# Optimization experiments

Hardware: AMD Instinct MI355X
Metric: run time of the kernel (lower is better)

## Reference

```python
import jax, jax.numpy as jnp
import numpy as np

B = 4          # batch_size (config.batch_size)
N = 17000      # num_prots (nodes per graph)
F_IN = 256     # num_features
C = 128        # out_channels
E = 2176000    # num edges (avg degree 32)
NODES = B * N


def _gcn_layer(x, W, b, src, dst, n):
    """PyG GCNConv: add self-loops, sym-normalized aggregation, then bias.
    out[i] = sum_{j->i} d_j^{-1/2} d_i^{-1/2} (x_j W) + d_i^{-1} (x_i W) + b
    with d = degree(dst) + 1 (self loop)."""
    h = x @ W  # [n, C]
    deg = jax.ops.segment_sum(jnp.ones(src.shape[0], x.dtype), dst, num_segments=n) + 1.0
    dinv = jax.lax.rsqrt(deg)  # [n]
    coef = dinv[src] * dinv[dst]                      # [E]
    agg = jax.ops.segment_sum(h[src] * coef[:, None], dst, num_segments=n)
    agg = agg + h * (dinv * dinv)[:, None]            # self-loop term
    return agg + b


def setup_inputs() -> dict:
    key = jax.random.key(0)
    ks = jax.random.split(key, 16)

    def glorot(k, shape):
        fan_in, fan_out = shape[0], shape[1]
        s = jnp.sqrt(6.0 / (fan_in + fan_out))
        return jax.random.uniform(k, shape, jnp.float32, -s, s)

    inp = {
        "x": jax.random.normal(ks[0], (NODES, F_IN), jnp.float32),
        "edge_index": jax.random.randint(ks[1], (2, E), 0, NODES, jnp.int32),
        "protein_mask": jax.random.randint(ks[2], (B, N), 0, 2, jnp.int32),
        "W1": glorot(ks[3], (F_IN, C)), "b1": jnp.zeros((C,), jnp.float32),
        "W2": glorot(ks[4], (C, C)),    "b2": jnp.zeros((C,), jnp.float32),
        "W3": glorot(ks[5], (C, C)),    "b3": jnp.zeros((C,), jnp.float32),
        "lw1": glorot(ks[6], (C, 256)), "lb1": jnp.zeros((256,), jnp.float32),
        "lw2": glorot(ks[7], (256, 64)), "lb2": jnp.zeros((64,), jnp.float32),
        "lw3": glorot(ks[8], (64, 16)),  "lb3": jnp.zeros((16,), jnp.float32),
        "lw4": glorot(ks[9], (16, 1)),   "lb4": jnp.zeros((1,), jnp.float32),
    }
    return inp


def reference(x, edge_index, protein_mask, W1, b1, W2, b2, W3, b3,
              lw1, lb1, lw2, lb2, lw3, lb3, lw4, lb4):
    src, dst = edge_index[0], edge_index[1]
    h1 = jax.nn.relu(_gcn_layer(x, W1, b1, src, dst, NODES))   # [NODES, C]
    h2 = jax.nn.relu(_gcn_layer(h1, W2, b2, src, dst, NODES))
    h3 = jax.nn.relu(_gcn_layer(h2, W3, b3, src, dst, NODES))
    s = (h1 + h2 + h3).reshape(B, N, C)                        # residual sum
    mask = protein_mask.astype(jnp.float32)                    # [B, N]
    pooled = jnp.einsum('bn,bnc->bc', mask, s)                 # masked bmm pool [B, C]
    z = jax.nn.relu(pooled @ lw1 + lb1)
    z = jax.nn.relu(z @ lw2 + lb2)
    z = jax.nn.relu(z @ lw3 + lb3)
    return z @ lw4 + lb4                                       # [B, 1]
```

## Files before the change

kernel.cpp:

```cpp
#include <hip/hip_runtime.h>
#include <hip/hip_bf16.h>
#include <cstdint>

#define F_IN 256
#define C 128
#define NBUK_MAX 320
#define CHUNK 4096
#define CAP 12288

typedef short bf8_t __attribute__((ext_vector_type(8)));
typedef float f4_t  __attribute__((ext_vector_type(4)));

static inline size_t align256(size_t x) { return (x + 255) & ~(size_t)255; }

static __device__ inline unsigned pack_bf16(float a, float b) {
    __hip_bfloat162 h = __float22bfloat162_rn(make_float2(a, b));
    return *(unsigned*)&h;
}

static __device__ inline bf8_t pack8(float4 u0, float4 u1) {
    union { unsigned u[4]; bf8_t v; } r;
    r.u[0] = pack_bf16(u0.x, u0.y);
    r.u[1] = pack_bf16(u0.z, u0.w);
    r.u[2] = pack_bf16(u1.x, u1.y);
    r.u[3] = pack_bf16(u1.z, u1.w);
    return r.v;
}

__global__ __launch_bounds__(256) void part_gemm1_kernel(
        const int* __restrict__ src, const int* __restrict__ dst,
        int* __restrict__ cntb, int* __restrict__ ebuf, int E, int nblk_part,
        const float* __restrict__ X, const __hip_bfloat16* __restrict__ Wsw,
        __hip_bfloat16* __restrict__ G, int M) {
    __shared__ __align__(16) char smem[36864];
    const int tid = threadIdx.x;

    if ((int)blockIdx.x < nblk_part) {
        int* hist = (int*)smem;
        int* base = hist + NBUK_MAX;
        int* gbase = base + NBUK_MAX;
        int2* stage = (int2*)(smem + 4096);
        const int e0 = blockIdx.x * CHUNK;
        const int cnt = min(CHUNK, E - e0);

        for (int i = tid; i < NBUK_MAX; i += 256) hist[i] = 0;
        __syncthreads();

        int2 ev[CHUNK / 256];
        int mo[CHUNK / 256];
#pragma unroll
        for (int k = 0; k < CHUNK / 256; ++k) {
            int e = e0 + k * 256 + tid;
            if (e < E) {
                int2 v;
                v.x = src[e];
                v.y = dst[e];
                ev[k] = v;
                mo[k] = atomicAdd(&hist[v.y >> 8], 1);
            }
        }
        __syncthreads();
        if (tid < 64) {
            int acc[5];
            int s = 0;
#pragma unroll
            for (int j = 0; j < 5; ++j) {
                acc[j] = s;
                s += hist[tid * 5 + j];
            }
            int tot = s;
#pragma unroll
            for (int d = 1; d < 64; d <<= 1) {
                int o = __shfl_up(tot, d);
                if (tid >= d) tot += o;
            }
            int excl = tot - s;
#pragma unroll
            for (int j = 0; j < 5; ++j) base[tid * 5 + j] = excl + acc[j];
        }
        __syncthreads();
        for (int i = tid; i < NBUK_MAX; i += 256) {
            int h = hist[i];
            gbase[i] = h ? atomicAdd(&cntb[i], h) : 0;
        }
        __syncthreads();
#pragma unroll
        for (int k = 0; k < CHUNK / 256; ++k) {
            int e = e0 + k * 256 + tid;
            if (e < E) stage[base[ev[k].y >> 8] + mo[k]] = ev[k];
        }
        __syncthreads();
        for (int i = tid; i < cnt; i += 256) {
            int2 e = stage[i];
            int b = e.y >> 8;
            ebuf[(size_t)b * CAP + gbase[b] + (i - base[b])] = ((e.y & 255) << 24) | e.x;
        }
    } else {
        char* lds = smem;
        const int gb = blockIdx.x - nblk_part;
        const int l = tid & 63;
        const int w = tid >> 6;
        const int lm = l & 15;
        const int lk = (l >> 4) * 8;
        const int row0 = gb * 128 + w * 32;
        const int K = F_IN;

        f4_t acc[2][8] = {};
        const float* xf[2];
#pragma unroll
        for (int mt = 0; mt < 2; ++mt) {
            int r = min(row0 + mt * 16 + lm, M - 1);
            xf[mt] = X + (size_t)r * K + lk;
        }
        float4 cf[2][2];
#pragma unroll
        for (int mt = 0; mt < 2; ++mt) {
            cf[mt][0] = *(const float4*)(xf[mt]);
            cf[mt][1] = *(const float4*)(xf[mt] + 4);
        }
        for (int s = 0; s < 8; ++s) {
            if ((s & 3) == 0) {
                if (s) __syncthreads();
                const char* wsrc = (const char*)Wsw + (size_t)s * 8192;
                for (int o = tid * 16; o < 32768; o += 256 * 16)
                    *(uint4*)(lds + o) = *(const uint4*)(wsrc + o);
                __syncthreads();
            }
            float4 nf[2][2];
            if (s + 1 < 8) {
#pragma unroll
                for (int mt = 0; mt < 2; ++mt) {
                    nf[mt][0] = *(const float4*)(xf[mt] + (s + 1) * 32);
                    nf[mt][1] = *(const float4*)(xf[mt] + (s + 1) * 32 + 4);
                }
            }
            bf8_t a[2];
#pragma unroll
            for (int mt = 0; mt < 2; ++mt)
                a[mt] = pack8(cf[mt][0], cf[mt][1]);
            const char* bbase = lds + ((size_t)((s & 3) * 8) * 64 + l) * 16;
#pragma unroll
            for (int u = 0; u < 8; ++u) {
                bf8_t b = *(const bf8_t*)(bbase + (size_t)u * 64 * 16);
#pragma unroll
                for (int mt = 0; mt < 2; ++mt)
                    acc[mt][u] = __builtin_amdgcn_mfma_f32_16x16x32_bf16(a[mt], b, acc[mt][u], 0, 0, 0);
            }
#pragma unroll
            for (int mt = 0; mt < 2; ++mt) {
                cf[mt][0] = nf[mt][0];
                cf[mt][1] = nf[mt][1];
            }
        }
#pragma unroll
        for (int mt = 0; mt < 2; ++mt) {
            int rbase = row0 + mt * 16 + (l >> 4) * 4;
#pragma unroll
            for (int r = 0; r < 4; ++r) {
                int row = rbase + r;
                if (row < M) {
#pragma unroll
                    for (int u = 0; u < 8; ++u)
                        G[(size_t)row * C + u * 16 + lm] = __float2bfloat16(acc[mt][u][r]);
                }
            }
        }
    }
}

__global__ __launch_bounds__(256) void csr_build_kernel(const int* __restrict__ ebuf,
                                                        const int* __restrict__ cntb,
                                                        int nbuk,
                                                        int* __restrict__ offs,
                                                        float* __restrict__ dinv,
                                                        int* __restrict__ csr, int nodes) {
    __shared__ int hist[NBUK_MAX];
    __shared__ int basep[NBUK_MAX];
    __shared__ int deg[256];
    __shared__ int p[256];
    __shared__ int pre[257];
    __shared__ int cur[256];
    const int b = blockIdx.x;
    const int n0 = b << 8;
    const int ncnt = min(256, nodes - n0);
    const int tid = threadIdx.x;

    for (int bk = tid; bk < NBUK_MAX; bk += 256)
        hist[bk] = (bk < nbuk) ? cntb[bk] : 0;
    __syncthreads();
    if (tid < 64) {
        int acc[5];
        int s = 0;
#pragma unroll
        for (int j = 0; j < 5; ++j) {
            acc[j] = s;
            s += hist[tid * 5 + j];
        }
        int tot = s;
#pragma unroll
        for (int d = 1; d < 64; d <<= 1) {
            int o = __shfl_up(tot, d);
            if (tid >= d) tot += o;
        }
        int excl = tot - s;
#pragma unroll
        for (int j = 0; j < 5; ++j) basep[tid * 5 + j] = excl + acc[j];
    }
    __syncthreads();
    const int eb = basep[b];
    const int cntE = hist[b];
    const int* slab = ebuf + (size_t)b * CAP;

    deg[tid] = 0;
    __syncthreads();
    for (int k = tid; k < cntE; k += 256)
        atomicAdd(&deg[(unsigned)slab[k] >> 24], 1);
    __syncthreads();
    p[tid] = deg[tid];
    __syncthreads();
    for (int d = 1; d < 256; d <<= 1) {
        int v = (tid >= d) ? p[tid - d] : 0;
        __syncthreads();
        p[tid] += v;
        __syncthreads();
    }
    pre[tid + 1] = p[tid];
    if (tid == 0) pre[0] = 0;
    __syncthreads();

    for (int i = tid; i <= ncnt; i += 256)
        offs[n0 + i] = eb + pre[i] + n0 + i;
    if (tid < ncnt) {
        dinv[n0 + tid] = rsqrtf((float)(deg[tid] + 1));
        csr[eb + pre[tid] + n0 + tid] = n0 + tid;
    }
    cur[tid] = 0;
    __syncthreads();
    for (int k = tid; k < cntE; k += 256) {
        int v = slab[k];
        int loc = (unsigned)v >> 24;
        int q = atomicAdd(&cur[loc], 1);
        csr[eb + pre[loc] + n0 + loc + 1 + q] = v & 0xFFFFFF;
    }
}

static __device__ inline void swz_one(const float* __restrict__ W,
                                      __hip_bfloat16* __restrict__ Wsw, int i) {
    int l = i & 63;
    int u = (i >> 6) & 7;
    int t = i >> 9;
    int krow = t * 32 + (l >> 4) * 8;
    int col = u * 16 + (l & 15);
    unsigned packed[4];
#pragma unroll
    for (int j = 0; j < 4; ++j) {
        float a = W[(size_t)(krow + 2 * j) * C + col];
        float b = W[(size_t)(krow + 2 * j + 1) * C + col];
        packed[j] = pack_bf16(a, b);
    }
    uint4 o = make_uint4(packed[0], packed[1], packed[2], packed[3]);
    *(uint4*)(Wsw + (size_t)i * 8) = o;
}

__global__ __launch_bounds__(256) void wswz_all_kernel(const float* __restrict__ W1,
                                                       const float* __restrict__ W2,
                                                       const float* __restrict__ W3,
                                                       __hip_bfloat16* __restrict__ Wsw1,
                                                       __hip_bfloat16* __restrict__ Wsw2,
                                                       __hip_bfloat16* __restrict__ Wsw3) {
    int i = blockIdx.x * blockDim.x + threadIdx.x;
    if (i < 4096)      swz_one(W1, Wsw1, i);
    else if (i < 6144) swz_one(W2, Wsw2, i - 4096);
    else if (i < 8192) swz_one(W3, Wsw3, i - 6144);
}

__global__ __launch_bounds__(256) void mfma_gemm_kernel(const __hip_bfloat16* __restrict__ Xv,
                                                        const __hip_bfloat16* __restrict__ Wsw,
                                                        const float* __restrict__ dinv,
                                                        __hip_bfloat16* __restrict__ G,
                                                        int M) {
    __shared__ char lds[32768];
    const int tid = threadIdx.x;
    const int l = tid & 63;
    const int w = tid >> 6;
    const int lm = l & 15;
    const int lk = (l >> 4) * 8;
    const int row0 = blockIdx.x * 128 + w * 32;
    const int K = C;

    f4_t acc[2][8] = {};
    const __hip_bfloat16* xb[2];
#pragma unroll
    for (int mt = 0; mt < 2; ++mt) {
        int r = min(row0 + mt * 16 + lm, M - 1);
        xb[mt] = Xv + (size_t)r * K + lk;
    }
    bf8_t cb[2];
#pragma unroll
    for (int mt = 0; mt < 2; ++mt)
        cb[mt] = *(const bf8_t*)(xb[mt]);

    for (int o = tid * 16; o < 32768; o += 256 * 16)
        *(uint4*)(lds + o) = *(const uint4*)((const char*)Wsw + o);
    __syncthreads();

    for (int s = 0; s < 4; ++s) {
        bf8_t nb[2];
        if (s + 1 < 4) {
#pragma unroll
            for (int mt = 0; mt < 2; ++mt)
                nb[mt] = *(const bf8_t*)(xb[mt] + (s + 1) * 32);
        }
        const char* bbase = lds + ((size_t)(s * 8) * 64 + l) * 16;
#pragma unroll
        for (int u = 0; u < 8; ++u) {
            bf8_t b = *(const bf8_t*)(bbase + (size_t)u * 64 * 16);
#pragma unroll
            for (int mt = 0; mt < 2; ++mt)
                acc[mt][u] = __builtin_amdgcn_mfma_f32_16x16x32_bf16(cb[mt], b, acc[mt][u], 0, 0, 0);
        }
#pragma unroll
        for (int mt = 0; mt < 2; ++mt)
            cb[mt] = nb[mt];
    }

#pragma unroll
    for (int mt = 0; mt < 2; ++mt) {
        int rbase = row0 + mt * 16 + (l >> 4) * 4;
#pragma unroll
        for (int r = 0; r < 4; ++r) {
            int row = rbase + r;
            if (row < M) {
                float dv = dinv[row];
#pragma unroll
                for (int u = 0; u < 8; ++u) {
                    float v = acc[mt][u][r] * dv;
                    G[(size_t)row * C + u * 16 + lm] = __float2bfloat16(v);
                }
            }
        }
    }
}

static __device__ inline void unpack_add(uint4 v, float* acc) {
    const __hip_bfloat162* hh = (const __hip_bfloat162*)&v;
#pragma unroll
    for (int t = 0; t < 4; ++t) {
        float2 f = __bfloat1622float2(hh[t]);
        acc[2 * t]     += f.x;
        acc[2 * t + 1] += f.y;
    }
}

static __device__ inline void unpack_fma(uint4 v, float dv, float* acc) {
    const __hip_bfloat162* hh = (const __hip_bfloat162*)&v;
#pragma unroll
    for (int t = 0; t < 4; ++t) {
        float2 f = __bfloat1622float2(hh[t]);
        acc[2 * t]     = fmaf(f.x, dv, acc[2 * t]);
        acc[2 * t + 1] = fmaf(f.y, dv, acc[2 * t + 1]);
    }
}

template <bool SS>
static __device__ inline void gather_rows(const char* __restrict__ Gb,
                                          const int* __restrict__ csr,
                                          const float* __restrict__ dinv,
                                          int beg, int end, int l, int g,
                                          unsigned qoff, float* acc) {
    for (int base = beg; base < end; base += 64) {
        const int cnt = min(64, end - base);
        int myidx = (l < cnt) ? csr[base + l] : 0;
        float mydv = SS ? dinv[myidx] : 1.f;
        int j = 0;
        for (; j + 16 <= cnt; j += 16) {
            int i0 = __shfl(myidx, j + g);
            int i1 = __shfl(myidx, j + 4 + g);
            int i2 = __shfl(myidx, j + 8 + g);
            int i3 = __shfl(myidx, j + 12 + g);
            uint4 v0 = *(const uint4*)(Gb + (((unsigned)i0 << 8) | qoff));
            uint4 v1 = *(const uint4*)(Gb + (((unsigned)i1 << 8) | qoff));
            uint4 v2 = *(const uint4*)(Gb + (((unsigned)i2 << 8) | qoff));
            uint4 v3 = *(const uint4*)(Gb + (((unsigned)i3 << 8) | qoff));
            if (SS) {
                float d0 = __shfl(mydv, j + g);
                float d1 = __shfl(mydv, j + 4 + g);
                float d2 = __shfl(mydv, j + 8 + g);
                float d3 = __shfl(mydv, j + 12 + g);
                unpack_fma(v0, d0, acc); unpack_fma(v1, d1, acc);
                unpack_fma(v2, d2, acc); unpack_fma(v3, d3, acc);
            } else {
                unpack_add(v0, acc); unpack_add(v1, acc);
                unpack_add(v2, acc); unpack_add(v3, acc);
            }
        }
        if (j + 8 <= cnt) {
            int i0 = __shfl(myidx, j + g);
            int i1 = __shfl(myidx, j + 4 + g);
            uint4 v0 = *(const uint4*)(Gb + (((unsigned)i0 << 8) | qoff));
            uint4 v1 = *(const uint4*)(Gb + (((unsigned)i1 << 8) | qoff));
            if (SS) {
                float d0 = __shfl(mydv, j + g);
                float d1 = __shfl(mydv, j + 4 + g);
                unpack_fma(v0, d0, acc); unpack_fma(v1, d1, acc);
            } else {
                unpack_add(v0, acc); unpack_add(v1, acc);
            }
            j += 8;
        }
        for (; j < cnt; j += 4) {
            int i0 = __shfl(myidx, j + g);
            float sc = (j + g < cnt) ? 1.f : 0.f;
            if (SS) sc *= __shfl(mydv, j + g);
            uint4 v0 = *(const uint4*)(Gb + (((unsigned)i0 << 8) | qoff));
            unpack_fma(v0, sc, acc);
        }
    }
}

template <bool SS>
__global__ __launch_bounds__(256) void agg_kernel(const __hip_bfloat16* __restrict__ G,
                                                  const int* __restrict__ csr,
                                                  const int* __restrict__ offs,
                                                  const float* __restrict__ dinv,
                                                  const float* __restrict__ bias,
                                                  __hip_bfloat16* __restrict__ A, int nodes) {
    const int node = blockIdx.x * 4 + (threadIdx.x >> 6);
    if (node >= nodes) return;
    const int l = threadIdx.x & 63;
    const int g = l >> 4;
    const unsigned qoff = (l & 15) * 16;
    const int beg = offs[node], end = offs[node + 1];
    float acc[8] = {};
    gather_rows<SS>((const char*)G, csr, dinv, beg, end, l, g, qoff, acc);

#pragma unroll
    for (int t = 0; t < 8; ++t) {
        acc[t] += __shfl_xor(acc[t], 16);
        acc[t] += __shfl_xor(acc[t], 32);
    }

    const float d = dinv[node];
    if (g == 0) {
        float bb[8];
        *(float4*)bb       = *(const float4*)(bias + qoff / 2);
        *(float4*)(bb + 4) = *(const float4*)(bias + qoff / 2 + 4);
        unsigned pk[4];
#pragma unroll
        for (int t = 0; t < 4; ++t) {
            float x0 = fmaxf(fmaf(acc[2 * t],     d, bb[2 * t]),     0.f);
            float x1 = fmaxf(fmaf(acc[2 * t + 1], d, bb[2 * t + 1]), 0.f);
            pk[t] = pack_bf16(x0, x1);
        }
        *(uint4*)((char*)A + (size_t)node * 256 + qoff) = make_uint4(pk[0], pk[1], pk[2], pk[3]);
    }
}

__global__ __launch_bounds__(64) void pool3_kernel(const __hip_bfloat16* __restrict__ S1,
                                                   const __hip_bfloat16* __restrict__ S2,
                                                   const __hip_bfloat16* __restrict__ S3,
                                                   const int* __restrict__ mask,
                                                   float* __restrict__ pooled, int N) {
    const int b = blockIdx.y;
    const int n0 = blockIdx.x * 128;
    const int c0 = threadIdx.x * 2;
    const int lim = min(n0 + 128, N);
    float ax = 0.f, ay = 0.f;
    for (int n = n0; n < lim; ++n) {
        if (mask[b * N + n]) {
            size_t o = ((size_t)b * N + n) * C + c0;
            float2 f1 = __bfloat1622float2(*(const __hip_bfloat162*)(S1 + o));
            float2 f2 = __bfloat1622float2(*(const __hip_bfloat162*)(S2 + o));
            float2 f3 = __bfloat1622float2(*(const __hip_bfloat162*)(S3 + o));
            ax += f1.x + f2.x + f3.x;
            ay += f1.y + f2.y + f3.y;
        }
    }
    atomicAdd(&pooled[b * C + c0], ax);
    atomicAdd(&pooled[b * C + c0 + 1], ay);
}

__global__ __launch_bounds__(256) void mlp_kernel(const float* __restrict__ pooled,
        const float* __restrict__ lw1, const float* __restrict__ lb1,
        const float* __restrict__ lw2, const float* __restrict__ lb2,
        const float* __restrict__ lw3, const float* __restrict__ lb3,
        const float* __restrict__ lw4, const float* __restrict__ lb4,
        float* __restrict__ out) {
    __shared__ float p[4 * 128];
    __shared__ float z1[4 * 256];
    __shared__ float z2[4 * 64];
    __shared__ float z3[4 * 16];
    const int tid = threadIdx.x;
    for (int i = tid; i < 4 * 128; i += 256) p[i] = pooled[i];
    __syncthreads();
    for (int o = tid; o < 4 * 256; o += 256) {
        int b = o >> 8, j = o & 255;
        float s = lb1[j];
        for (int k = 0; k < 128; ++k) s += p[b * 128 + k] * lw1[k * 256 + j];
        z1[o] = fmaxf(s, 0.f);
    }
    __syncthreads();
    for (int o = tid; o < 4 * 64; o += 256) {
        int b = o >> 6, j = o & 63;
        float s = lb2[j];
        for (int k = 0; k < 256; ++k) s += z1[b * 256 + k] * lw2[k * 64 + j];
        z2[o] = fmaxf(s, 0.f);
    }
    __syncthreads();
    if (tid < 64) {
        int b = tid >> 4, j = tid & 15;
        float s = lb3[j];
        for (int k = 0; k < 64; ++k) s += z2[b * 64 + k] * lw3[k * 16 + j];
        z3[tid] = fmaxf(s, 0.f);
    }
    __syncthreads();
    if (tid < 4) {
        float s = lb4[0];
        for (int k = 0; k < 16; ++k) s += z3[tid * 16 + k] * lw4[k];
        out[tid] = s;
    }
}


extern "C" void kernel_launch(void* const* d_in, const int* in_sizes, int n_in,
                              void* d_out, int out_size, void* d_ws, size_t ws_size,
                              hipStream_t stream) {
    const float* x    = (const float*)d_in[0];
    const int*   ei   = (const int*)d_in[1];
    const int*   pmask = (const int*)d_in[2];
    const float* W1 = (const float*)d_in[3];  const float* b1 = (const float*)d_in[4];
    const float* W2 = (const float*)d_in[5];  const float* b2 = (const float*)d_in[6];
    const float* W3 = (const float*)d_in[7];  const float* b3 = (const float*)d_in[8];
    const float* lw1 = (const float*)d_in[9];  const float* lb1 = (const float*)d_in[10];
    const float* lw2 = (const float*)d_in[11]; const float* lb2 = (const float*)d_in[12];
    const float* lw3 = (const float*)d_in[13]; const float* lb3 = (const float*)d_in[14];
    const float* lw4 = (const float*)d_in[15]; const float* lb4 = (const float*)d_in[16];
    float* out = (float*)d_out;

    const int E = in_sizes[1] / 2;
    const int NODES = in_sizes[0] / F_IN;
    const int NB = 4;
    const int NPER = NODES / NB;
    const int NBUK = (NODES + 255) >> 8;
    const int NBLK = (E + CHUNK - 1) / CHUNK;
    const int* esrc = ei;
    const int* edst = ei + E;

    char* w = (char*)d_ws;
    size_t off = 0;
    auto alloc = [&](size_t bytes) -> void* {
        void* p = w + off;
        off = align256(off + bytes);
        return p;
    };
    float* dinv = (float*)alloc((size_t)NODES * 4);
    int*   offs = (int*)  alloc((size_t)(NODES + 1) * 4);
    int*   cntb = (int*)  alloc((size_t)NBUK * 4);
    int*   ebuf = (int*)  alloc((size_t)NBUK * CAP * 4);
    int*   csr  = (int*)  alloc((size_t)(E + NODES) * 4);
    __hip_bfloat16* G   = (__hip_bfloat16*)alloc((size_t)NODES * C * 2);
    __hip_bfloat16* A1  = (__hip_bfloat16*)alloc((size_t)NODES * C * 2);
    __hip_bfloat16* A2  = (__hip_bfloat16*)alloc((size_t)NODES * C * 2);
    __hip_bfloat16* A3  = (__hip_bfloat16*)alloc((size_t)NODES * C * 2);
    __hip_bfloat16* Wsw1 = (__hip_bfloat16*)alloc((size_t)F_IN * C * 2);
    __hip_bfloat16* Wsw2 = (__hip_bfloat16*)alloc((size_t)C * C * 2);
    __hip_bfloat16* Wsw3 = (__hip_bfloat16*)alloc((size_t)C * C * 2);
    float* pooled = (float*)alloc((size_t)4 * C * 4);
    (void)ws_size; (void)n_in; (void)out_size;

    hipMemsetAsync(cntb,   0, (size_t)NBUK * 4, stream);
    hipMemsetAsync(pooled, 0, (size_t)4 * C * 4, stream);

    const int gblocks128 = (NODES + 127) / 128;
    const int ablocks = (NODES + 3) / 4;

    wswz_all_kernel<<<32, 256, 0, stream>>>(W1, W2, W3, Wsw1, Wsw2, Wsw3);

    part_gemm1_kernel<<<NBLK + gblocks128, 256, 0, stream>>>(
        esrc, edst, cntb, ebuf, E, NBLK, x, Wsw1, G, NODES);

    csr_build_kernel<<<NBUK, 256, 0, stream>>>(ebuf, cntb, NBUK, offs, dinv, csr, NODES);

    agg_kernel<true><<<ablocks, 256, 0, stream>>>(G, csr, offs, dinv, b1, A1, NODES);
    mfma_gemm_kernel<<<gblocks128, 256, 0, stream>>>(A1, Wsw2, dinv, G, NODES);
    agg_kernel<false><<<ablocks, 256, 0, stream>>>(G, csr, offs, dinv, b2, A2, NODES);
    mfma_gemm_kernel<<<gblocks128, 256, 0, stream>>>(A2, Wsw3, dinv, G, NODES);
    agg_kernel<false><<<ablocks, 256, 0, stream>>>(G, csr, offs, dinv, b3, A3, NODES);

    dim3 pgrid((NPER + 127) / 128, NB);
    pool3_kernel<<<pgrid, 64, 0, stream>>>(A1, A2, A3, pmask, pooled, NPER);
    mlp_kernel<<<1, 256, 0, stream>>>(pooled, lw1, lb1, lw2, lb2, lw3, lb3, lw4, lb4, out);
}
```

Baseline: 480.0 us.

## Split layers into halves and overlap aggregation with next GEMM via union kernels

Each GCN layer's node range is split into two halves. The first half's aggregation runs alone. The second half's aggregation then runs in the same launch as the next layer's GEMM over the first half, and the remaining GEMM blocks run afterwards. G is double-buffered (GA/GB) so a GEMM can write while aggregation still reads the other buffer. Pooling of layers 1 and 2 now runs inside the final aggregation launch, which leaves a lighter single-tensor pool for layer 3. The GEMM's LDS staging drops to 16KB in two chunks to raise occupancy, at the cost of an extra barrier and more kernel launches.

Measured after the change: 570.7 us. 1.19x slower.

```diff
diff --git a/kernel.cpp b/kernel.cpp
--- a/kernel.cpp
+++ b/kernel.cpp
@@ -146,10 +146,12 @@
                 for (int mt = 0; mt < 2; ++mt)
                     acc[mt][u] = __builtin_amdgcn_mfma_f32_16x16x32_bf16(a[mt], b, acc[mt][u], 0, 0, 0);
             }
-#pragma unroll
-            for (int mt = 0; mt < 2; ++mt) {
-                cf[mt][0] = nf[mt][0];
-                cf[mt][1] = nf[mt][1];
+            if (s + 1 < 8) {
+#pragma unroll
+                for (int mt = 0; mt < 2; ++mt) {
+                    cf[mt][0] = nf[mt][0];
+                    cf[mt][1] = nf[mt][1];
+                }
             }
         }
 #pragma unroll
@@ -274,54 +276,56 @@
     else if (i < 8192) swz_one(W3, Wsw3, i - 6144);
 }
 
-__global__ __launch_bounds__(256) void mfma_gemm_kernel(const __hip_bfloat16* __restrict__ Xv,
-                                                        const __hip_bfloat16* __restrict__ Wsw,
-                                                        const float* __restrict__ dinv,
-                                                        __hip_bfloat16* __restrict__ G,
-                                                        int M) {
-    __shared__ char lds[32768];
-    const int tid = threadIdx.x;
+static __device__ inline void gemm128_body(const __hip_bfloat16* __restrict__ Xv,
+                                           const __hip_bfloat16* __restrict__ Wsw,
+                                           const float* __restrict__ dinv,
+                                           __hip_bfloat16* __restrict__ G2,
+                                           int M, int row0blk, int tid, char* lds) {
     const int l = tid & 63;
     const int w = tid >> 6;
     const int lm = l & 15;
     const int lk = (l >> 4) * 8;
-    const int row0 = blockIdx.x * 128 + w * 32;
-    const int K = C;
+    const int row0 = row0blk + w * 32;
 
     f4_t acc[2][8] = {};
     const __hip_bfloat16* xb[2];
 #pragma unroll
     for (int mt = 0; mt < 2; ++mt) {
         int r = min(row0 + mt * 16 + lm, M - 1);
-        xb[mt] = Xv + (size_t)r * K + lk;
+        xb[mt] = Xv + (size_t)r * C + lk;
     }
     bf8_t cb[2];
 #pragma unroll
     for (int mt = 0; mt < 2; ++mt)
         cb[mt] = *(const bf8_t*)(xb[mt]);
 
-    for (int o = tid * 16; o < 32768; o += 256 * 16)
-        *(uint4*)(lds + o) = *(const uint4*)((const char*)Wsw + o);
-    __syncthreads();
-
-    for (int s = 0; s < 4; ++s) {
-        bf8_t nb[2];
-        if (s + 1 < 4) {
-#pragma unroll
-            for (int mt = 0; mt < 2; ++mt)
-                nb[mt] = *(const bf8_t*)(xb[mt] + (s + 1) * 32);
-        }
-        const char* bbase = lds + ((size_t)(s * 8) * 64 + l) * 16;
-#pragma unroll
-        for (int u = 0; u < 8; ++u) {
-            bf8_t b = *(const bf8_t*)(bbase + (size_t)u * 64 * 16);
-#pragma unroll
-            for (int mt = 0; mt < 2; ++mt)
-                acc[mt][u] = __builtin_amdgcn_mfma_f32_16x16x32_bf16(cb[mt], b, acc[mt][u], 0, 0, 0);
-        }
-#pragma unroll
-        for (int mt = 0; mt < 2; ++mt)
-            cb[mt] = nb[mt];
+    for (int c = 0; c < 2; ++c) {
+        if (c) __syncthreads();
+        for (int o = tid * 16; o < 16384; o += 256 * 16)
+            *(uint4*)(lds + o) = *(const uint4*)((const char*)Wsw + (size_t)c * 16384 + o);
+        __syncthreads();
+        for (int s2 = 0; s2 < 2; ++s2) {
+            const int s = c * 2 + s2;
+            bf8_t nb[2];
+            if (s + 1 < 4) {
+#pragma unroll
+                for (int mt = 0; mt < 2; ++mt)
+                    nb[mt] = *(const bf8_t*)(xb[mt] + (s + 1) * 32);
+            }
+            const char* bbase = lds + ((size_t)(s2 * 8) * 64 + l) * 16;
+#pragma unroll
+            for (int u = 0; u < 8; ++u) {
+                bf8_t b = *(const bf8_t*)(bbase + (size_t)u * 64 * 16);
+#pragma unroll
+                for (int mt = 0; mt < 2; ++mt)
+                    acc[mt][u] = __builtin_amdgcn_mfma_f32_16x16x32_bf16(cb[mt], b, acc[mt][u], 0, 0, 0);
+            }
+            if (s + 1 < 4) {
+#pragma unroll
+                for (int mt = 0; mt < 2; ++mt)
+                    cb[mt] = nb[mt];
+            }
+        }
     }
 
 #pragma unroll
@@ -335,11 +339,20 @@
 #pragma unroll
                 for (int u = 0; u < 8; ++u) {
                     float v = acc[mt][u][r] * dv;
-                    G[(size_t)row * C + u * 16 + lm] = __float2bfloat16(v);
+                    G2[(size_t)row * C + u * 16 + lm] = __float2bfloat16(v);
                 }
             }
         }
     }
+}
+
+__global__ __launch_bounds__(256) void mfma_gemm_kernel(const __hip_bfloat16* __restrict__ Xv,
+                                                        const __hip_bfloat16* __restrict__ Wsw,
+                                                        const float* __restrict__ dinv,
+                                                        __hip_bfloat16* __restrict__ G2,
+                                                        int rowBase, int M) {
+    __shared__ __align__(16) char lds[16384];
+    gemm128_body(Xv, Wsw, dinv, G2, M, rowBase + blockIdx.x * 128, threadIdx.x, lds);
 }
 
 static __device__ inline void unpack_add(uint4 v, float* acc) {
@@ -419,15 +432,14 @@
 }
 
 template <bool SS>
-__global__ __launch_bounds__(256) void agg_kernel(const __hip_bfloat16* __restrict__ G,
-                                                  const int* __restrict__ csr,
-                                                  const int* __restrict__ offs,
-                                                  const float* __restrict__ dinv,
-                                                  const float* __restrict__ bias,
-                                                  __hip_bfloat16* __restrict__ A, int nodes) {
-    const int node = blockIdx.x * 4 + (threadIdx.x >> 6);
-    if (node >= nodes) return;
-    const int l = threadIdx.x & 63;
+static __device__ inline void agg_node_body(const __hip_bfloat16* __restrict__ G,
+                                            const int* __restrict__ csr,
+                                            const int* __restrict__ offs,
+                                            const float* __restrict__ dinv,
+                                            const float* __restrict__ bias,
+                                            __hip_bfloat16* __restrict__ A,
+                                            int node, int tid) {
+    const int l = tid & 63;
     const int g = l >> 4;
     const unsigned qoff = (l & 15) * 16;
     const int beg = offs[node], end = offs[node + 1];
@@ -456,9 +468,76 @@
     }
 }
 
-__global__ __launch_bounds__(64) void pool3_kernel(const __hip_bfloat16* __restrict__ S1,
-                                                   const __hip_bfloat16* __restrict__ S2,
-                                                   const __hip_bfloat16* __restrict__ S3,
+template <bool SS>
+__global__ __launch_bounds__(256) void agg_kernel(const __hip_bfloat16* __restrict__ G,
+                                                  const int* __restrict__ csr,
+                                                  const int* __restrict__ offs,
+                                                  const float* __restrict__ dinv,
+                                                  const float* __restrict__ bias,
+                                                  __hip_bfloat16* __restrict__ A,
+                                                  int nodeBase, int nodes) {
+    const int node = nodeBase + blockIdx.x * 4 + (threadIdx.x >> 6);
+    if (node >= nodes) return;
+    agg_node_body<SS>(G, csr, offs, dinv, bias, A, node, threadIdx.x);
+}
+
+template <bool SS>
+__global__ __launch_bounds__(256) void agg_gemm_union_kernel(
+        const __hip_bfloat16* __restrict__ Gsrc,
+        const int* __restrict__ csr, const int* __restrict__ offs,
+        const float* __restrict__ dinv, const float* __restrict__ bias,
+        __hip_bfloat16* __restrict__ A, int nodeBase, int nodes, int nAggBlk,
+        const __hip_bfloat16* __restrict__ Xv, const __hip_bfloat16* __restrict__ Wsw,
+        __hip_bfloat16* __restrict__ Gdst) {
+    __shared__ __align__(16) char lds[16384];
+    const int tid = threadIdx.x;
+    if ((int)blockIdx.x < nAggBlk) {
+        const int node = nodeBase + blockIdx.x * 4 + (tid >> 6);
+        if (node >= nodes) return;
+        agg_node_body<SS>(Gsrc, csr, offs, dinv, bias, A, node, tid);
+    } else {
+        const int gb = blockIdx.x - nAggBlk;
+        gemm128_body(Xv, Wsw, dinv, Gdst, nodes, gb * 128, tid, lds);
+    }
+}
+
+__global__ __launch_bounds__(256) void agg_pool12_union_kernel(
+        const __hip_bfloat16* __restrict__ Gsrc,
+        const int* __restrict__ csr, const int* __restrict__ offs,
+        const float* __restrict__ dinv, const float* __restrict__ bias,
+        __hip_bfloat16* __restrict__ A3, int nodeBase, int nodes, int nAggBlk,
+        const __hip_bfloat16* __restrict__ S1, const __hip_bfloat16* __restrict__ S2,
+        const int* __restrict__ mask, float* __restrict__ pooled, int N, int nbx) {
+    const int tid = threadIdx.x;
+    if ((int)blockIdx.x < nAggBlk) {
+        const int node = nodeBase + blockIdx.x * 4 + (tid >> 6);
+        if (node >= nodes) return;
+        agg_node_body<false>(Gsrc, csr, offs, dinv, bias, A3, node, tid);
+    } else {
+        const int pb = blockIdx.x - nAggBlk;
+        const int bx = pb % nbx;
+        const int by = pb / nbx;
+        const int l = tid & 63;
+        const int w = tid >> 6;
+        const int c0 = l * 2;
+        const int n0 = bx * 128;
+        const int lim = min(n0 + 128, N);
+        float ax = 0.f, ay = 0.f;
+        for (int n = n0 + w; n < lim; n += 4) {
+            if (mask[by * N + n]) {
+                size_t o = ((size_t)by * N + n) * C + c0;
+                float2 f1 = __bfloat1622float2(*(const __hip_bfloat162*)(S1 + o));
+                float2 f2 = __bfloat1622float2(*(const __hip_bfloat162*)(S2 + o));
+                ax += f1.x + f2.x;
+                ay += f1.y + f2.y;
+            }
+        }
+        atomicAdd(&pooled[by * C + c0], ax);
+        atomicAdd(&pooled[by * C + c0 + 1], ay);
+    }
+}
+
+__global__ __launch_bounds__(64) void pool1_kernel(const __hip_bfloat16* __restrict__ S,
                                                    const int* __restrict__ mask,
                                                    float* __restrict__ pooled, int N) {
     const int b = blockIdx.y;
@@ -469,11 +548,9 @@
     for (int n = n0; n < lim; ++n) {
         if (mask[b * N + n]) {
             size_t o = ((size_t)b * N + n) * C + c0;
-            float2 f1 = __bfloat1622float2(*(const __hip_bfloat162*)(S1 + o));
-            float2 f2 = __bfloat1622float2(*(const __hip_bfloat162*)(S2 + o));
-            float2 f3 = __bfloat1622float2(*(const __hip_bfloat162*)(S3 + o));
-            ax += f1.x + f2.x + f3.x;
-            ay += f1.y + f2.y + f3.y;
+            float2 f = __bfloat1622float2(*(const __hip_bfloat162*)(S + o));
+            ax += f.x;
+            ay += f.y;
         }
     }
     atomicAdd(&pooled[b * C + c0], ax);
@@ -558,7 +635,8 @@
     int*   cntb = (int*)  alloc((size_t)NBUK * 4);
     int*   ebuf = (int*)  alloc((size_t)NBUK * CAP * 4);
     int*   csr  = (int*)  alloc((size_t)(E + NODES) * 4);
-    __hip_bfloat16* G   = (__hip_bfloat16*)alloc((size_t)NODES * C * 2);
+    __hip_bfloat16* GA  = (__hip_bfloat16*)alloc((size_t)NODES * C * 2);
+    __hip_bfloat16* GB  = (__hip_bfloat16*)alloc((size_t)NODES * C * 2);
     __hip_bfloat16* A1  = (__hip_bfloat16*)alloc((size_t)NODES * C * 2);
     __hip_bfloat16* A2  = (__hip_bfloat16*)alloc((size_t)NODES * C * 2);
     __hip_bfloat16* A3  = (__hip_bfloat16*)alloc((size_t)NODES * C * 2);
@@ -571,23 +649,36 @@
     hipMemsetAsync(cntb,   0, (size_t)NBUK * 4, stream);
     hipMemsetAsync(pooled, 0, (size_t)4 * C * 4, stream);
 
-    const int gblocks128 = (NODES + 127) / 128;
-    const int ablocks = (NODES + 3) / 4;
+    const int gbl = (NODES + 127) / 128;
+    const int gA  = gbl / 2;
+    const int H   = min(gA * 128, NODES);
+    const int gB  = gbl - gA;
+    const int aggA = (H + 3) / 4;
+    const int aggB = (NODES - H + 3) / 4;
+    const int nbx = (NPER + 127) / 128;
 
     wswz_all_kernel<<<32, 256, 0, stream>>>(W1, W2, W3, Wsw1, Wsw2, Wsw3);
 
-    part_gemm1_kernel<<<NBLK + gblocks128, 256, 0, stream>>>(
-        esrc, edst, cntb, ebuf, E, NBLK, x, Wsw1, G, NODES);
+    part_gemm1_kernel<<<NBLK + gbl, 256, 0, stream>>>(
+        esrc, edst, cntb, ebuf, E, NBLK, x, Wsw1, GA, NODES);
 
     csr_build_kernel<<<NBUK, 256, 0, stream>>>(ebuf, cntb, NBUK, offs, dinv, csr, NODES);
 
-    agg_kernel<true><<<ablocks, 256, 0, stream>>>(G, csr, offs, dinv, b1, A1, NODES);
-    mfma_gemm_kernel<<<gblocks128, 256, 0, stream>>>(A1, Wsw2, dinv, G, NODES);
-    agg_kernel<false><<<ablocks, 256, 0, stream>>>(G, csr, offs, dinv, b2, A2, NODES);
-    mfma_gemm_kernel<<<gblocks128, 256, 0, stream>>>(A2, Wsw3, dinv, G, NODES);
-    agg_kernel<false><<<ablocks, 256, 0, stream>>>(G, csr, offs, dinv, b3, A3, NODES);
-
-    dim3 pgrid((NPER + 127) / 128, NB);
-    pool3_kernel<<<pgrid, 64, 0, stream>>>(A1, A2, A3, pmask, pooled, NPER);
+    agg_kernel<true><<<aggA, 256, 0, stream>>>(GA, csr, offs, dinv, b1, A1, 0, NODES);
+    agg_gemm_union_kernel<true><<<aggB + gA, 256, 0, stream>>>(
+        GA, csr, offs, dinv, b1, A1, H, NODES, aggB, A1, Wsw2, GB);
+    mfma_gemm_kernel<<<gB, 256, 0, stream>>>(A1, Wsw2, dinv, GB, H, NODES);
+
+    agg_kernel<false><<<aggA, 256, 0, stream>>>(GB, csr, offs, dinv, b2, A2, 0, NODES);
+    agg_gemm_union_kernel<false><<<aggB + gA, 256, 0, stream>>>(
+        GB, csr, offs, dinv, b2, A2, H, NODES, aggB, A2, Wsw3, GA);
+    mfma_gemm_kernel<<<gB, 256, 0, stream>>>(A2, Wsw3, dinv, GA, H, NODES);
+
+    agg_kernel<false><<<aggA, 256, 0, stream>>>(GA, csr, offs, dinv, b3, A3, 0, NODES);
+    agg_pool12_union_kernel<<<aggB + nbx * NB, 256, 0, stream>>>(
+        GA, csr, offs, dinv, b3, A3, H, NODES, aggB, A1, A2, pmask, pooled, NPER, nbx);
+
+    dim3 pgrid(nbx, NB);
+    pool1_kernel<<<pgrid, 64, 0, stream>>>(A3, pmask, pooled, NPER);
     mlp_kernel<<<1, 256, 0, stream>>>(pooled, lw1, lb1, lw2, lb2, lw3, lb3, lw4, lb4, out);
 }
```
